# Kernel tuning notes

Measured on AMD Instinct MI355X. Metric: run time of the kernel, lower is better.

The kernel has to match this reference:

```python
import jax, jax.numpy as jnp
import numpy as np

B, N, E, H = 2, 512, 128, 256
IN_DIM = 3 * E + 1


def setup_inputs() -> dict:
    key = jax.random.key(0)
    ks = jax.random.split(key, 9)
    node_embed = jax.random.normal(ks[0], (B, N, E), dtype=jnp.float32)
    problems = jax.random.uniform(ks[1], (B, N, 4), dtype=jnp.float32)
    euclid = jax.random.uniform(ks[2], (B, N, N), dtype=jnp.float32)
    euclid = 0.5 * (euclid + jnp.swapaxes(euclid, 1, 2))  # symmetric, realistic
    s = 0.02
    W1 = s * jax.random.normal(ks[3], (IN_DIM, H), dtype=jnp.float32)
    b1 = jnp.zeros((H,), jnp.float32)
    W2 = s * jax.random.normal(ks[4], (H, H), dtype=jnp.float32)
    b2 = jnp.zeros((H,), jnp.float32)
    W3 = s * jax.random.normal(ks[5], (H, 1), dtype=jnp.float32)
    b3 = jnp.zeros((1,), jnp.float32)
    return {"node_embed": node_embed, "problems": problems,
            "euclid_distance_matrix": euclid,
            "W1": W1, "b1": b1, "W2": W2, "b2": b2, "W3": W3, "b3": b3}


def _forward(node_embed, euclid, W1, b1, W2, b2, W3, b3):
    b, n, e = node_embed.shape
    hi = jnp.broadcast_to(node_embed[:, :, None, :], (b, n, n, e))
    hj = jnp.broadcast_to(node_embed[:, None, :, :], (b, n, n, e))
    habs = jnp.abs(node_embed[:, :, None, :] - node_embed[:, None, :, :])
    x = jnp.concatenate([hi, hj, habs, euclid[..., None]], axis=-1)  # (B,N,N,3E+1)
    h = jax.nn.relu(jnp.einsum('bijf,fh->bijh', x, W1) + b1)
    h = jax.nn.relu(jnp.einsum('bijh,hg->bijg', h, W2) + b2)
    pred = (jnp.einsum('bijh,ho->bijo', h, W3) + b3)[..., 0]  # (B,N,N)
    pred = 0.5 * (pred + jnp.swapaxes(pred, 1, 2))
    pred = pred * (1.0 - jnp.eye(n, dtype=pred.dtype))  # zero diagonal
    return pred


def reference(node_embed, problems, euclid_distance_matrix, W1, b1, W2, b2, W3, b3):
    # euclid_distance_matrix provided, so `problems` fallback path is unused
    return _forward(node_embed, euclid_distance_matrix, W1, b1, W2, b2, W3, b3)
```

## Files before the change

### kernel.cpp

```cpp
#include <hip/hip_runtime.h>
#include <hip/hip_bf16.h>


#define BN 512
#define EE 128
#define HH 256
#define TJ 128

typedef __attribute__((ext_vector_type(8)))  short short8;
typedef __attribute__((ext_vector_type(4)))  short short4v;
typedef __attribute__((ext_vector_type(16))) float f32x16;
typedef __attribute__((ext_vector_type(4)))  float f32x4;

static __device__ __forceinline__ unsigned short f2bf(float f) {
    __bf16 h = (__bf16)f;
    return __builtin_bit_cast(unsigned short, h);
}
static __device__ __forceinline__ f32x16 zero16() {
    f32x16 v;
    #pragma unroll
    for (int i = 0; i < 16; ++i) v[i] = 0.f;
    return v;
}
#define MFMA(a, b, c) __builtin_amdgcn_mfma_f32_32x32x16_bf16((a), (b), (c), 0, 0, 0)

__global__ void prep(const float* __restrict__ node, const float* __restrict__ W1,
                     const float* __restrict__ W2, const float* __restrict__ b1,
                     float* __restrict__ PA, float* __restrict__ PBT,
                     unsigned short* __restrict__ w1c_p, unsigned short* __restrict__ w2_p) {
    int blk = blockIdx.x;
    if (blk < 256) {
        int idx = blk * 256 + threadIdx.x;
        int t = idx & 7, l = (idx >> 3) & 63, mt = (idx >> 9) & 7, kb = idx >> 12;
        int k = kb * 16 + (l >> 5) * 8 + t, m = mt * 32 + (l & 31);
        w2_p[idx] = f2bf(W2[k * HH + m]);
        if (idx < 32768)
            w1c_p[idx] = f2bf(W1[(2 * EE + k) * HH + m]);
    } else {
        int bi0 = (blk - 256) * 4;
        int h = threadIdx.x;
        float sa[4], sb[4];
        #pragma unroll
        for (int n = 0; n < 4; ++n) { sa[n] = b1[h]; sb[n] = 0.f; }
        #pragma unroll 8
        for (int e = 0; e < EE; ++e) {
            float wa = W1[e * HH + h];
            float wb = W1[(EE + e) * HH + h];
            #pragma unroll
            for (int n = 0; n < 4; ++n) {
                float nv = node[(size_t)(bi0 + n) * EE + e];
                sa[n] += nv * wa;
                sb[n] += nv * wb;
            }
        }
        #pragma unroll
        for (int n = 0; n < 4; ++n) {
            int bi = bi0 + n;
            PA[(size_t)bi * HH + h] = sa[n];
            PBT[(((size_t)(bi >> 9) * 64 + (h >> 2)) * BN + (bi & 511)) * 4 + (h & 3)] = sb[n];
        }
    }
}

__global__ __launch_bounds__(512, 4) void edge_main(
    const float* __restrict__ node, const float* __restrict__ euclid,
    const float* __restrict__ W1, const float* __restrict__ W3,
    const float* __restrict__ b3, const float* __restrict__ b2v,
    const float* __restrict__ PA, const float* __restrict__ PBT,
    const unsigned short* __restrict__ w1c_p, const unsigned short* __restrict__ w2_p,
    float* __restrict__ out)
{
    __shared__ __align__(16) unsigned short lds_buf[TJ * 264];
    __shared__ float pp[512];

    const int jt = blockIdx.x, i = blockIdx.y, b = blockIdx.z;
    const int jbase = jt * TJ;
    const int tid = threadIdx.x, wave = tid >> 6, lane = tid & 63;
    const int m0 = lane & 31, q = lane >> 5;
    const int wm = wave & 3, wn = wave >> 2;

    unsigned short* ldsD  = lds_buf;
    unsigned short* ldsH1 = lds_buf;

    const float* erow = euclid + ((size_t)b * BN + i) * BN + jbase;
    float ev[2];
    #pragma unroll
    for (int nt = 0; nt < 2; ++nt) ev[nt] = erow[(wn * 2 + nt) * 32 + m0];

    {
        int row = tid >> 2, q4 = tid & 3;
        const f32x4* nj = (const f32x4*)(node + ((size_t)b * BN + jbase + row) * EE);
        const f32x4* hv = (const f32x4*)(node + ((size_t)b * BN + i) * EE);
        #pragma unroll
        for (int g = 0; g < 4; ++g) {
            int c0 = q4 * 8 + g * 2;
            f32x4 a0 = nj[c0], a1 = nj[c0 + 1];
            f32x4 h0 = hv[c0], h1v = hv[c0 + 1];
            short8 pd;
            #pragma unroll
            for (int u = 0; u < 4; ++u) {
                pd[u]     = (short)f2bf(fabsf(a0[u] - h0[u]));
                pd[4 + u] = (short)f2bf(fabsf(a1[u] - h1v[u]));
            }
            *(short8*)&ldsD[row * 136 + q4 * 32 + g * 8] = pd;
        }
    }
    __syncthreads();

    f32x16 acc[2][2];
    #pragma unroll
    for (int mt = 0; mt < 2; ++mt)
        #pragma unroll
        for (int nt = 0; nt < 2; ++nt) acc[mt][nt] = zero16();
    {
        const short8* wc = (const short8*)w1c_p;
        #pragma unroll
        for (int kb = 0; kb < 8; ++kb) {
            short8 ac0 = wc[(kb * 8 + wm * 2 + 0) * 64 + lane];
            short8 ac1 = wc[(kb * 8 + wm * 2 + 1) * 64 + lane];
            #pragma unroll
            for (int nt = 0; nt < 2; ++nt) {
                short8 bD = *(const short8*)&ldsD[((wn * 2 + nt) * 32 + m0) * 136 + kb * 16 + q * 8];
                acc[0][nt] = MFMA(ac0, bD, acc[0][nt]);
                acc[1][nt] = MFMA(ac1, bD, acc[1][nt]);
            }
        }
    }
    __syncthreads();

    {
        const float* paB = PA + ((size_t)b * BN + i) * HH;
        const float* wd  = W1 + (size_t)(3 * EE) * HH;
        const float* pbt = PBT + (size_t)b * 64 * BN * 4;
        #pragma unroll
        for (int mt = 0; mt < 2; ++mt) {
            #pragma unroll
            for (int rg = 0; rg < 4; ++rg) {
                int f0 = (wm * 2 + mt) * 32 + rg * 8;
                f32x4 plo = *(const f32x4*)&paB[f0];
                f32x4 phi = *(const f32x4*)&paB[f0 + 4];
                f32x4 dlo = *(const f32x4*)&wd[f0];
                f32x4 dhi = *(const f32x4*)&wd[f0 + 4];
                #pragma unroll
                for (int nt = 0; nt < 2; ++nt) {
                    f32x4 pbv = *(const f32x4*)&pbt[
                        (((size_t)(f0 >> 2) + q) * BN + jbase + (wn * 2 + nt) * 32 + m0) * 4];
                    short4v w;
                    #pragma unroll
                    for (int u = 0; u < 4; ++u) {
                        float pav = q ? phi[u] : plo[u];
                        float wdv = q ? dhi[u] : dlo[u];
                        float v = acc[mt][nt][rg * 4 + u] + pav + pbv[u] + ev[nt] * wdv;
                        v = v > 0.f ? v : 0.f;
                        w[u] = (short)f2bf(v);
                    }
                    *(short4v*)&ldsH1[((wn * 2 + nt) * 32 + m0) * 264 + f0 + 4 * q] = w;
                }
            }
        }
    }
    __syncthreads();

    f32x16 c2[2][2];
    #pragma unroll
    for (int mt = 0; mt < 2; ++mt)
        #pragma unroll
        for (int nt = 0; nt < 2; ++nt) c2[mt][nt] = zero16();
    {
        const short8* w2f = (const short8*)w2_p;
        #pragma unroll
        for (int kb = 0; kb < 16; ++kb) {
            short8 a0 = w2f[(kb * 8 + wm * 2 + 0) * 64 + lane];
            short8 a1 = w2f[(kb * 8 + wm * 2 + 1) * 64 + lane];
            #pragma unroll
            for (int nt = 0; nt < 2; ++nt) {
                short8 bh = *(const short8*)&ldsH1[((wn * 2 + nt) * 32 + m0) * 264 + kb * 16 + q * 8];
                c2[0][nt] = MFMA(a0, bh, c2[0][nt]);
                c2[1][nt] = MFMA(a1, bh, c2[1][nt]);
            }
        }
    }

    {
        float s[2] = {0.f, 0.f};
        #pragma unroll
        for (int mt = 0; mt < 2; ++mt) {
            #pragma unroll
            for (int rg = 0; rg < 4; ++rg) {
                int f0 = (wm * 2 + mt) * 32 + rg * 8;
                f32x4 blo = *(const f32x4*)&b2v[f0];
                f32x4 bhi = *(const f32x4*)&b2v[f0 + 4];
                f32x4 wlo = *(const f32x4*)&W3[f0];
                f32x4 whi = *(const f32x4*)&W3[f0 + 4];
                #pragma unroll
                for (int u = 0; u < 4; ++u) {
                    float bb = q ? bhi[u] : blo[u];
                    float ww = q ? whi[u] : wlo[u];
                    #pragma unroll
                    for (int nt = 0; nt < 2; ++nt) {
                        float h2 = c2[mt][nt][rg * 4 + u] + bb;
                        h2 = h2 > 0.f ? h2 : 0.f;
                        s[nt] += h2 * ww;
                    }
                }
            }
        }
        #pragma unroll
        for (int nt = 0; nt < 2; ++nt)
            s[nt] += __shfl_xor(s[nt], 32, 64);
        if (lane < 32) {
            #pragma unroll
            for (int nt = 0; nt < 2; ++nt)
                pp[(wave * 2 + nt) * 32 + lane] = s[nt];
        }
    }
    __syncthreads();
    if (tid < TJ) {
        int wn2 = tid >> 6, nt = (tid >> 5) & 1, l5 = tid & 31;
        float v = b3[0];
        #pragma unroll
        for (int wm2 = 0; wm2 < 4; ++wm2)
            v += pp[(((wn2 * 4 + wm2) * 2) + nt) * 32 + l5];
        out[((size_t)b * BN + i) * BN + jbase + tid] = v;
    }
}

__global__ void symmetrize(float* __restrict__ out) {
    int b = blockIdx.z, ti = blockIdx.y, tj = blockIdx.x;
    if (tj < ti) return;
    int i = ti * 32 + threadIdx.y, j = tj * 32 + threadIdx.x;
    float* p = out + (size_t)b * BN * BN;
    if (i == j) { p[(size_t)i * BN + j] = 0.f; return; }
    if (j < i) return;
    float a = p[(size_t)i * BN + j];
    float c = p[(size_t)j * BN + i];
    float v = 0.5f * (a + c);
    p[(size_t)i * BN + j] = v;
    p[(size_t)j * BN + i] = v;
}

extern "C" void kernel_launch(void* const* d_in, const int* in_sizes, int n_in,
                              void* d_out, int out_size, void* d_ws, size_t ws_size,
                              hipStream_t stream) {
    const float* node   = (const float*)d_in[0];
    const float* euclid = (const float*)d_in[2];
    const float* W1     = (const float*)d_in[3];
    const float* b1     = (const float*)d_in[4];
    const float* W2     = (const float*)d_in[5];
    const float* b2     = (const float*)d_in[6];
    const float* W3     = (const float*)d_in[7];
    const float* b3     = (const float*)d_in[8];
    float* out = (float*)d_out;

    char* ws = (char*)d_ws;
    float*          PA    = (float*)ws;
    float*          PBT   = (float*)(ws + (1u << 20));
    unsigned short* w1c_p = (unsigned short*)(ws + (2u << 20));
    unsigned short* w2_p  = (unsigned short*)(ws + (2u << 20) + 65536);

    prep<<<512, 256, 0, stream>>>(node, W1, W2, b1, PA, PBT, w1c_p, w2_p);
    edge_main<<<dim3(BN / TJ, BN, 2), 512, 0, stream>>>(
        node, euclid, W1, W3, b3, b2, PA, PBT, w1c_p, w2_p, out);
    symmetrize<<<dim3(BN / 32, BN / 32, 2), dim3(32, 32), 0, stream>>>(out);
}
```

Before: 272.5 us.

## Loop each block over four j-tiles with double-buffered diff tile and register-held W1 fragments

The edge kernel now uses 256-thread blocks that each process four 64-wide j tiles in sequence, rather than one 128-wide tile per 512-thread block. The |h_i - h_j| tile for the next j tile is loaded and converted into a second LDS buffer while the current tile is being computed. The W1 diff-weight fragments and the h_i row are loaded once into registers and reused across the tiles. This cuts repeated global weight loads and some barrier stalls, but it raises register pressure and halves the number of blocks, which may lower occupancy.

```diff
diff --git a/kernel.cpp b/kernel.cpp
--- a/kernel.cpp
+++ b/kernel.cpp
@@ -5,7 +5,7 @@
 #define BN 512
 #define EE 128
 #define HH 256
-#define TJ 128
+#define TJ 64
 
 typedef __attribute__((ext_vector_type(8)))  short short8;
 typedef __attribute__((ext_vector_type(4)))  short short4v;
@@ -62,7 +62,7 @@
     }
 }
 
-__global__ __launch_bounds__(512, 4) void edge_main(
+__global__ __launch_bounds__(256, 2) void edge_main(
     const float* __restrict__ node, const float* __restrict__ euclid,
     const float* __restrict__ W1, const float* __restrict__ W3,
     const float* __restrict__ b3, const float* __restrict__ b2v,
@@ -70,73 +70,87 @@
     const unsigned short* __restrict__ w1c_p, const unsigned short* __restrict__ w2_p,
     float* __restrict__ out)
 {
-    __shared__ __align__(16) unsigned short lds_buf[TJ * 264];
-    __shared__ float pp[512];
-
-    const int jt = blockIdx.x, i = blockIdx.y, b = blockIdx.z;
-    const int jbase = jt * TJ;
+    __shared__ __align__(16) unsigned short ldsD[2][TJ * 136];
+    __shared__ __align__(16) unsigned short ldsH1[TJ * 264];
+    __shared__ float pp[256];
+
+    const int jg = blockIdx.x, i = blockIdx.y, b = blockIdx.z;
     const int tid = threadIdx.x, wave = tid >> 6, lane = tid & 63;
     const int m0 = lane & 31, q = lane >> 5;
-    const int wm = wave & 3, wn = wave >> 2;
-
-    unsigned short* ldsD  = lds_buf;
-    unsigned short* ldsH1 = lds_buf;
-
-    const float* erow = euclid + ((size_t)b * BN + i) * BN + jbase;
-    float ev[2];
+    const int row = tid >> 2, q4 = tid & 3;
+
+    const f32x4* hv = (const f32x4*)(node + ((size_t)b * BN + i) * EE);
+    f32x4 hi[8];
     #pragma unroll
-    for (int nt = 0; nt < 2; ++nt) ev[nt] = erow[(wn * 2 + nt) * 32 + m0];
-
+    for (int c = 0; c < 8; ++c) hi[c] = hv[q4 * 8 + c];
+
+    short8 wcf[2][8];
     {
-        int row = tid >> 2, q4 = tid & 3;
+        const short8* wcp = (const short8*)w1c_p;
+        #pragma unroll
+        for (int kb = 0; kb < 8; ++kb) {
+            wcf[0][kb] = wcp[(kb * 8 + wave * 2 + 0) * 64 + lane];
+            wcf[1][kb] = wcp[(kb * 8 + wave * 2 + 1) * 64 + lane];
+        }
+    }
+
+    const float* erow = euclid + ((size_t)b * BN + i) * BN;
+    const float* paB  = PA + ((size_t)b * BN + i) * HH;
+    const float* wd   = W1 + (size_t)(3 * EE) * HH;
+    const float* pbt  = PBT + (size_t)b * 64 * BN * 4;
+    const short8* w2f = (const short8*)w2_p;
+
+    int jbase = jg * 4 * TJ;
+    {
         const f32x4* nj = (const f32x4*)(node + ((size_t)b * BN + jbase + row) * EE);
-        const f32x4* hv = (const f32x4*)(node + ((size_t)b * BN + i) * EE);
+        f32x4 jr[8];
+        #pragma unroll
+        for (int c = 0; c < 8; ++c) jr[c] = nj[q4 * 8 + c];
         #pragma unroll
         for (int g = 0; g < 4; ++g) {
-            int c0 = q4 * 8 + g * 2;
-            f32x4 a0 = nj[c0], a1 = nj[c0 + 1];
-            f32x4 h0 = hv[c0], h1v = hv[c0 + 1];
             short8 pd;
             #pragma unroll
             for (int u = 0; u < 4; ++u) {
-                pd[u]     = (short)f2bf(fabsf(a0[u] - h0[u]));
-                pd[4 + u] = (short)f2bf(fabsf(a1[u] - h1v[u]));
-            }
-            *(short8*)&ldsD[row * 136 + q4 * 32 + g * 8] = pd;
+                pd[u]     = (short)f2bf(fabsf(jr[g * 2][u]     - hi[g * 2][u]));
+                pd[4 + u] = (short)f2bf(fabsf(jr[g * 2 + 1][u] - hi[g * 2 + 1][u]));
+            }
+            *(short8*)&ldsD[0][row * 136 + q4 * 32 + g * 8] = pd;
         }
     }
     __syncthreads();
 
-    f32x16 acc[2][2];
-    #pragma unroll
-    for (int mt = 0; mt < 2; ++mt)
-        #pragma unroll
-        for (int nt = 0; nt < 2; ++nt) acc[mt][nt] = zero16();
-    {
-        const short8* wc = (const short8*)w1c_p;
+    int cur = 0;
+    for (int t = 0; t < 4; ++t, jbase += TJ) {
+        f32x4 jn[8];
+        if (t < 3) {
+            const f32x4* nj = (const f32x4*)(node + ((size_t)b * BN + jbase + TJ + row) * EE);
+            #pragma unroll
+            for (int c = 0; c < 8; ++c) jn[c] = nj[q4 * 8 + c];
+        }
+        float ev[2];
+        #pragma unroll
+        for (int nt = 0; nt < 2; ++nt) ev[nt] = erow[jbase + nt * 32 + m0];
+
+        f32x16 acc[2][2];
+        #pragma unroll
+        for (int mt = 0; mt < 2; ++mt)
+            #pragma unroll
+            for (int nt = 0; nt < 2; ++nt) acc[mt][nt] = zero16();
         #pragma unroll
         for (int kb = 0; kb < 8; ++kb) {
-            short8 ac0 = wc[(kb * 8 + wm * 2 + 0) * 64 + lane];
-            short8 ac1 = wc[(kb * 8 + wm * 2 + 1) * 64 + lane];
             #pragma unroll
             for (int nt = 0; nt < 2; ++nt) {
-                short8 bD = *(const short8*)&ldsD[((wn * 2 + nt) * 32 + m0) * 136 + kb * 16 + q * 8];
-                acc[0][nt] = MFMA(ac0, bD, acc[0][nt]);
-                acc[1][nt] = MFMA(ac1, bD, acc[1][nt]);
-            }
-        }
-    }
-    __syncthreads();
-
-    {
-        const float* paB = PA + ((size_t)b * BN + i) * HH;
-        const float* wd  = W1 + (size_t)(3 * EE) * HH;
-        const float* pbt = PBT + (size_t)b * 64 * BN * 4;
+                short8 bD = *(const short8*)&ldsD[cur][(nt * 32 + m0) * 136 + kb * 16 + q * 8];
+                acc[0][nt] = MFMA(wcf[0][kb], bD, acc[0][nt]);
+                acc[1][nt] = MFMA(wcf[1][kb], bD, acc[1][nt]);
+            }
+        }
+
         #pragma unroll
         for (int mt = 0; mt < 2; ++mt) {
             #pragma unroll
             for (int rg = 0; rg < 4; ++rg) {
-                int f0 = (wm * 2 + mt) * 32 + rg * 8;
+                int f0 = (wave * 2 + mt) * 32 + rg * 8;
                 f32x4 plo = *(const f32x4*)&paB[f0];
                 f32x4 phi = *(const f32x4*)&paB[f0 + 4];
                 f32x4 dlo = *(const f32x4*)&wd[f0];
@@ -144,7 +158,7 @@
                 #pragma unroll
                 for (int nt = 0; nt < 2; ++nt) {
                     f32x4 pbv = *(const f32x4*)&pbt[
-                        (((size_t)(f0 >> 2) + q) * BN + jbase + (wn * 2 + nt) * 32 + m0) * 4];
+                        (((size_t)(f0 >> 2) + q) * BN + jbase + nt * 32 + m0) * 4];
                     short4v w;
                     #pragma unroll
                     for (int u = 0; u < 4; ++u) {
@@ -154,74 +168,85 @@
                         v = v > 0.f ? v : 0.f;
                         w[u] = (short)f2bf(v);
                     }
-                    *(short4v*)&ldsH1[((wn * 2 + nt) * 32 + m0) * 264 + f0 + 4 * q] = w;
+                    *(short4v*)&ldsH1[(nt * 32 + m0) * 264 + f0 + 4 * q] = w;
                 }
             }
         }
-    }
-    __syncthreads();
-
-    f32x16 c2[2][2];
-    #pragma unroll
-    for (int mt = 0; mt < 2; ++mt)
-        #pragma unroll
-        for (int nt = 0; nt < 2; ++nt) c2[mt][nt] = zero16();
-    {
-        const short8* w2f = (const short8*)w2_p;
+
+        if (t < 3) {
+            #pragma unroll
+            for (int g = 0; g < 4; ++g) {
+                short8 pd;
+                #pragma unroll
+                for (int u = 0; u < 4; ++u) {
+                    pd[u]     = (short)f2bf(fabsf(jn[g * 2][u]     - hi[g * 2][u]));
+                    pd[4 + u] = (short)f2bf(fabsf(jn[g * 2 + 1][u] - hi[g * 2 + 1][u]));
+                }
+                *(short8*)&ldsD[cur ^ 1][row * 136 + q4 * 32 + g * 8] = pd;
+            }
+        }
+        __syncthreads();
+
+        f32x16 c2[2][2];
+        #pragma unroll
+        for (int mt = 0; mt < 2; ++mt)
+            #pragma unroll
+            for (int nt = 0; nt < 2; ++nt) c2[mt][nt] = zero16();
         #pragma unroll
         for (int kb = 0; kb < 16; ++kb) {
-            short8 a0 = w2f[(kb * 8 + wm * 2 + 0) * 64 + lane];
-            short8 a1 = w2f[(kb * 8 + wm * 2 + 1) * 64 + lane];
+            short8 a0 = w2f[(kb * 8 + wave * 2 + 0) * 64 + lane];
+            short8 a1 = w2f[(kb * 8 + wave * 2 + 1) * 64 + lane];
             #pragma unroll
             for (int nt = 0; nt < 2; ++nt) {
-                short8 bh = *(const short8*)&ldsH1[((wn * 2 + nt) * 32 + m0) * 264 + kb * 16 + q * 8];
+                short8 bh = *(const short8*)&ldsH1[(nt * 32 + m0) * 264 + kb * 16 + q * 8];
                 c2[0][nt] = MFMA(a0, bh, c2[0][nt]);
                 c2[1][nt] = MFMA(a1, bh, c2[1][nt]);
             }
         }
-    }
-
-    {
-        float s[2] = {0.f, 0.f};
-        #pragma unroll
-        for (int mt = 0; mt < 2; ++mt) {
-            #pragma unroll
-            for (int rg = 0; rg < 4; ++rg) {
-                int f0 = (wm * 2 + mt) * 32 + rg * 8;
-                f32x4 blo = *(const f32x4*)&b2v[f0];
-                f32x4 bhi = *(const f32x4*)&b2v[f0 + 4];
-                f32x4 wlo = *(const f32x4*)&W3[f0];
-                f32x4 whi = *(const f32x4*)&W3[f0 + 4];
-                #pragma unroll
-                for (int u = 0; u < 4; ++u) {
-                    float bb = q ? bhi[u] : blo[u];
-                    float ww = q ? whi[u] : wlo[u];
+
+        {
+            float s[2] = {0.f, 0.f};
+            #pragma unroll
+            for (int mt = 0; mt < 2; ++mt) {
+                #pragma unroll
+                for (int rg = 0; rg < 4; ++rg) {
+                    int f0 = (wave * 2 + mt) * 32 + rg * 8;
+                    f32x4 blo = *(const f32x4*)&b2v[f0];
+                    f32x4 bhi = *(const f32x4*)&b2v[f0 + 4];
+                    f32x4 wlo = *(const f32x4*)&W3[f0];
+                    f32x4 whi = *(const f32x4*)&W3[f0 + 4];
                     #pragma unroll
-                    for (int nt = 0; nt < 2; ++nt) {
-                        float h2 = c2[mt][nt][rg * 4 + u] + bb;
-                        h2 = h2 > 0.f ? h2 : 0.f;
-                        s[nt] += h2 * ww;
+                    for (int u = 0; u < 4; ++u) {
+                        float bb = q ? bhi[u] : blo[u];
+                        float ww = q ? whi[u] : wlo[u];
+                        #pragma unroll
+                        for (int nt = 0; nt < 2; ++nt) {
+                            float h2 = c2[mt][nt][rg * 4 + u] + bb;
+                            h2 = h2 > 0.f ? h2 : 0.f;
+                            s[nt] += h2 * ww;
+                        }
                     }
                 }
             }
-        }
-        #pragma unroll
-        for (int nt = 0; nt < 2; ++nt)
-            s[nt] += __shfl_xor(s[nt], 32, 64);
-        if (lane < 32) {
             #pragma unroll
             for (int nt = 0; nt < 2; ++nt)
-                pp[(wave * 2 + nt) * 32 + lane] = s[nt];
-        }
-    }
-    __syncthreads();
-    if (tid < TJ) {
-        int wn2 = tid >> 6, nt = (tid >> 5) & 1, l5 = tid & 31;
-        float v = b3[0];
-        #pragma unroll
-        for (int wm2 = 0; wm2 < 4; ++wm2)
-            v += pp[(((wn2 * 4 + wm2) * 2) + nt) * 32 + l5];
-        out[((size_t)b * BN + i) * BN + jbase + tid] = v;
+                s[nt] += __shfl_xor(s[nt], 32, 64);
+            if (lane < 32) {
+                #pragma unroll
+                for (int nt = 0; nt < 2; ++nt)
+                    pp[(wave * 2 + nt) * 32 + lane] = s[nt];
+            }
+        }
+        __syncthreads();
+        if (tid < TJ) {
+            int nt = tid >> 5, l5 = tid & 31;
+            float v = b3[0];
+            #pragma unroll
+            for (int wm = 0; wm < 4; ++wm)
+                v += pp[(wm * 2 + nt) * 32 + l5];
+            out[((size_t)b * BN + i) * BN + jbase + tid] = v;
+        }
+        cur ^= 1;
     }
 }
 
@@ -259,7 +284,7 @@
     unsigned short* w2_p  = (unsigned short*)(ws + (2u << 20) + 65536);
 
     prep<<<512, 256, 0, stream>>>(node, W1, W2, b1, PA, PBT, w1c_p, w2_p);
-    edge_main<<<dim3(BN / TJ, BN, 2), 512, 0, stream>>>(
+    edge_main<<<dim3(2, BN, 2), 256, 0, stream>>>(
         node, euclid, W1, W3, b3, b2, PA, PBT, w1c_p, w2_p, out);
     symmetrize<<<dim3(BN / 32, BN / 32, 2), dim3(32, 32), 0, stream>>>(out);
 }
```

Result: slower. 622.7 us (+128.5%).
